# Optimization experiments

Hardware: AMD Instinct MI355X
Metric: run time of the kernel (lower is better)

The kernel has to match this reference:

```python
import jax, jax.numpy as jnp
import numpy as np

ROUTER_FEATS = 32  # per perspective

def setup_inputs() -> dict:
    key = jax.random.key(0)
    ks = jax.random.split(key, 8)
    B, L1, L2, L3, E = 16384, 3072, 15, 32, 8
    x = jax.random.normal(ks[0], (B, L1), dtype=jnp.float32)
    router_w = jax.random.normal(ks[1], (E, 2 * ROUTER_FEATS), dtype=jnp.float32) * 0.1
    router_b = jnp.zeros((E,), dtype=jnp.float32)
    l1_w = jax.random.normal(ks[2], (E, L2 + 1, L1), dtype=jnp.float32) / np.sqrt(L1)
    l1_b = jax.random.normal(ks[3], (E, L2 + 1), dtype=jnp.float32) * 0.01
    l2_w = jax.random.normal(ks[4], (E, L3, 2 * L2), dtype=jnp.float32) / np.sqrt(2 * L2)
    l2_b = jax.random.normal(ks[5], (E, L3), dtype=jnp.float32) * 0.01
    out_w = jax.random.normal(ks[6], (E, 1, L3), dtype=jnp.float32) / np.sqrt(L3)
    out_b = jnp.zeros((E, 1), dtype=jnp.float32)
    return {"x": x, "router_w": router_w, "router_b": router_b,
            "l1_w": l1_w, "l1_b": l1_b, "l2_w": l2_w, "l2_b": l2_b,
            "out_w": out_w, "out_b": out_b}

def reference(x, router_w, router_b, l1_w, l1_b, l2_w, l2_b, out_w, out_b):
    # x: [B, L1]; l1_w: [E, L2+1, L1]; l2_w: [E, L3, 2*L2]; out_w: [E, 1, L3]
    L2 = l2_w.shape[2] // 2
    half = x.shape[1] // 2
    # router: first ROUTER_FEATS features of each perspective
    router_in = jnp.concatenate([x[:, :ROUTER_FEATS], x[:, half:half + ROUTER_FEATS]], axis=1)  # [B, 64]
    gate_logits = router_in @ router_w.T + router_b  # [B, E]
    expert_indices = jnp.argmax(gate_logits, axis=-1)  # [B]
    # all-experts dense forward
    l1c = jnp.einsum('bi,eoi->beo', x, l1_w) + l1_b          # [B, E, L2+1]
    l1x, l1x_out = l1c[..., :L2], l1c[..., L2:]               # [B,E,L2], [B,E,1]
    l1x = jnp.clip(jnp.concatenate([jnp.square(l1x) * (255.0 / 256.0), l1x], axis=2), 0.0, 1.0)  # [B,E,2*L2]
    l2c = jnp.einsum('bei,eoi->beo', l1x, l2_w) + l2_b        # [B, E, L3]
    l2x = jnp.clip(l2c, 0.0, 1.0)
    l3c = jnp.einsum('bei,eoi->beo', l2x, out_w) + out_b      # [B, E, 1]
    all_outputs = l3c + l1x_out                               # [B, E, 1]
    # gather selected expert output (eval path)
    out = jnp.take_along_axis(all_outputs, expert_indices[:, None, None], axis=1)[:, 0, :]  # [B, 1]
    return out
```

## Files before the change

### kernel.cpp

```cpp
#include <hip/hip_runtime.h>
#include <cstdint>
#include <cstddef>

#define NROWS   16384
#define L1DIM   3072
#define NEXP    8
#define NO1     16
#define NFEAT   30
#define NL3     32
#define RFEAT   32

#define RPB     32
#define KC      192
#define NCHUNK  16
#define PITCH   196
#define NKS     8
#define KSL     24
#define SENT    0x7FFFFFFF
#define RBLK    256
#define MAXSLOTS (NROWS + NEXP*RPB)
#define MBLK    (MAXSLOTS/RPB)

__device__ int g_eid[NROWS];
__device__ int g_bc[RBLK*NEXP];
__device__ int g_off[NEXP+1];
__device__ int g_cur[NEXP];
__device__ int g_bucket[MAXSLOTS];

__global__ __launch_bounds__(64) void k_router(const float* __restrict__ x,
                                               const float* __restrict__ rw,
                                               const float* __restrict__ rb){
  int tid = threadIdx.x;
  int row = blockIdx.x*64 + tid;
  const float* xr = x + (size_t)row * L1DIM;
  float rin[2*RFEAT];
  #pragma unroll
  for (int i=0;i<8;i++){
    float4 v = *(const float4*)(xr + i*4);
    rin[i*4+0]=v.x; rin[i*4+1]=v.y; rin[i*4+2]=v.z; rin[i*4+3]=v.w;
  }
  #pragma unroll
  for (int i=0;i<8;i++){
    float4 v = *(const float4*)(xr + (L1DIM/2) + i*4);
    rin[32+i*4+0]=v.x; rin[32+i*4+1]=v.y; rin[32+i*4+2]=v.z; rin[32+i*4+3]=v.w;
  }
  float best = -3.0e38f; int be = 0;
  #pragma unroll
  for (int e=0;e<NEXP;e++){
    float s = rb[e];
    #pragma unroll
    for (int i=0;i<64;i++) s += rin[i]*rw[e*64+i];
    if (s > best){ best = s; be = e; }
  }
  g_eid[row] = be;
  __shared__ int cnt[NEXP];
  if (tid < NEXP) cnt[tid] = 0;
  __syncthreads();
  atomicAdd(&cnt[be], 1);
  __syncthreads();
  if (tid < NEXP) g_bc[blockIdx.x*NEXP + tid] = cnt[tid];
}

__global__ __launch_bounds__(256) void k_offsets(){
  __shared__ int part[256];
  __shared__ int scnt[NEXP];
  __shared__ int soff[NEXP+1];
  int tid = threadIdx.x;
  {
    int e = tid & 7, grp = tid >> 3;
    int s = 0;
    for (int b = grp; b < RBLK; b += 32) s += g_bc[b*NEXP + e];
    part[tid] = s;
  }
  __syncthreads();
  if (tid < NEXP){
    int t = 0;
    #pragma unroll
    for (int g=0; g<32; g++) t += part[g*NEXP + tid];
    scnt[tid] = t;
    g_cur[tid] = 0;
  }
  __syncthreads();
  if (tid == 0){
    int o = 0;
    for (int ee=0; ee<NEXP; ee++){
      soff[ee] = o;
      o += ((scnt[ee] + RPB - 1) / RPB) * RPB;
    }
    soff[NEXP] = o;
    for (int i=0;i<=NEXP;i++) g_off[i] = soff[i];
  }
  __syncthreads();
  for (int ee=0; ee<NEXP; ee++){
    int s    = soff[ee] + scnt[ee];
    int epad = soff[ee+1];
    for (int i = s + tid; i < epad; i += 256) g_bucket[i] = SENT;
  }
}

__global__ __launch_bounds__(64) void k_scatter(){
  int lane = threadIdx.x;
  int row = blockIdx.x*64 + lane;
  int e = g_eid[row];
  unsigned long long peers = 0;
  #pragma unroll
  for (int j=0;j<NEXP;j++){
    unsigned long long m = __ballot(e == j);
    if (e == j) peers = m;
  }
  int rank   = __popcll(peers & ((1ull << lane) - 1ull));
  int leader = __ffsll((unsigned long long)peers) - 1;
  int base = 0;
  if (lane == leader) base = atomicAdd(&g_cur[e], __popcll(peers));
  base = __shfl(base, leader, 64);
  g_bucket[g_off[e] + base + rank] = row;
}

__global__ __launch_bounds__(256,2) void k_main(const float* __restrict__ x,
    const float* __restrict__ l1w, const float* __restrict__ l1b,
    const float* __restrict__ l2w, const float* __restrict__ l2b,
    const float* __restrict__ ow,  const float* __restrict__ ob,
    float* __restrict__ out){
  __shared__ __align__(16) float sX[RPB][PITCH];
  __shared__ __align__(16) float sW[NO1][PITCH];
  __shared__ int sRows[RPB];
  __shared__ int sE;

  int tid = threadIdx.x;
  int slot0 = blockIdx.x * RPB;
  if (tid == 0){
    int e = -1;
    if (slot0 < g_off[NEXP]){
      #pragma unroll
      for (int j=0;j<NEXP;j++) if (slot0 >= g_off[j] && slot0 < g_off[j+1]) e = j;
    }
    sE = e;
  }
  __syncthreads();
  int e = sE;
  if (e < 0) return;
  if (tid < RPB) sRows[tid] = g_bucket[slot0 + tid];

  int ks = tid >> 5;
  int l5 = tid & 31;
  int og = l5 & 3;
  int rg = l5 >> 2;

  float acc[4][4];
  #pragma unroll
  for (int i=0;i<4;i++)
    #pragma unroll
    for (int j=0;j<4;j++) acc[i][j] = 0.f;

  const float* we = l1w + (size_t)e * (NO1 * L1DIM);

  for (int c=0;c<NCHUNK;c++){
    int kb = c * KC;
    __syncthreads();
    #pragma unroll
    for (int p=0;p<6;p++){
      int i = tid + p*256;
      int r = i / (KC/4), k4 = i % (KC/4);
      int gr = sRows[r];
      if (gr == SENT) gr = 0;
      float4 v = *(const float4*)(x + (size_t)gr * L1DIM + kb + k4*4);
      *(float4*)(&sX[r][k4*4]) = v;
    }
    #pragma unroll
    for (int p=0;p<3;p++){
      int i = tid + p*256;
      int o = i / (KC/4), k4 = i % (KC/4);
      float4 v = *(const float4*)(we + (size_t)o * L1DIM + kb + k4*4);
      *(float4*)(&sW[o][k4*4]) = v;
    }
    __syncthreads();
    int k0 = ks * KSL;
    #pragma unroll
    for (int q=0;q<KSL/4;q++){
      int k = k0 + q*4;
      float4 xv[4], wv[4];
      #pragma unroll
      for (int i=0;i<4;i++) xv[i] = *(const float4*)(&sX[rg + i*8][k]);
      #pragma unroll
      for (int j=0;j<4;j++) wv[j] = *(const float4*)(&sW[og + j*4][k]);
      #pragma unroll
      for (int ri=0;ri<4;ri++)
        #pragma unroll
        for (int oi=0;oi<4;oi++){
          acc[ri][oi] += xv[ri].x * wv[oi].x;
          acc[ri][oi] += xv[ri].y * wv[oi].y;
          acc[ri][oi] += xv[ri].z * wv[oi].z;
          acc[ri][oi] += xv[ri].w * wv[oi].w;
        }
    }
  }

  __syncthreads();
  float* red = &sX[0][0];
  #pragma unroll
  for (int ri=0;ri<4;ri++)
    #pragma unroll
    for (int oi=0;oi<4;oi++)
      red[(ks*RPB + (rg + ri*8))*17 + (og + oi*4)] = acc[ri][oi];
  __syncthreads();

  if (tid < RPB*4){
    int row = tid >> 2;
    int g   = tid & 3;
    float l1c[NO1];
    #pragma unroll
    for (int j=0;j<NO1;j++){
      float s = l1b[e*NO1 + j];
      #pragma unroll
      for (int sl=0;sl<NKS;sl++) s += red[(sl*RPB + row)*17 + j];
      l1c[j] = s;
    }
    float feat[NFEAT];
    #pragma unroll
    for (int j=0;j<15;j++){
      float v = l1c[j];
      feat[j]    = fminf(v*v*(255.0f/256.0f), 1.0f);
      feat[15+j] = fminf(fmaxf(v, 0.0f), 1.0f);
    }
    float l1xout = l1c[15];
    const float* w2 = l2w + e*NL3*NFEAT;
    const float* wo = ow  + e*NL3;
    float acc3 = 0.f;
    #pragma unroll
    for (int oo=0;oo<8;oo++){
      int o = g*8 + oo;
      float s = l2b[e*NL3 + o];
      #pragma unroll
      for (int i=0;i<NFEAT;i++) s += feat[i]*w2[o*NFEAT + i];
      s = fminf(fmaxf(s, 0.0f), 1.0f);
      acc3 += s * wo[o];
    }
    acc3 += __shfl_xor(acc3, 1);
    acc3 += __shfl_xor(acc3, 2);
    if (g == 0){
      int grow = sRows[row];
      if (grow != SENT) out[grow] = acc3 + ob[e] + l1xout;
    }
  }
}

extern "C" void kernel_launch(void* const* d_in, const int* in_sizes, int n_in,
                              void* d_out, int out_size, void* d_ws, size_t ws_size,
                              hipStream_t stream){
  (void)in_sizes; (void)n_in; (void)d_ws; (void)ws_size; (void)out_size;
  const float* x   = (const float*)d_in[0];
  const float* rw  = (const float*)d_in[1];
  const float* rb  = (const float*)d_in[2];
  const float* l1w = (const float*)d_in[3];
  const float* l1b = (const float*)d_in[4];
  const float* l2w = (const float*)d_in[5];
  const float* l2b = (const float*)d_in[6];
  const float* ow  = (const float*)d_in[7];
  const float* ob  = (const float*)d_in[8];
  float* out = (float*)d_out;

  hipLaunchKernelGGL(k_router,  dim3(RBLK), dim3(64),  0, stream, x, rw, rb);
  hipLaunchKernelGGL(k_offsets, dim3(1),    dim3(256), 0, stream);
  hipLaunchKernelGGL(k_scatter, dim3(RBLK), dim3(64),  0, stream);
  hipLaunchKernelGGL(k_main,    dim3(MBLK), dim3(256), 0, stream,
                     x, l1w, l1b, l2w, l2b, ow, ob, out);
}
```

Measured before the change: 341.2 us.

## Double-buffer main GEMM tiles via register prefetch; replace scatter atomics with prefix scan

k_main now keeps two shared-memory buffers and loads the next K-chunk of x and weights into registers while the current chunk is being multiplied. This hides global-load latency and cuts one barrier per chunk. Gather offsets are precomputed once and __launch_bounds__ loses the min-blocks hint. Separately, k_offsets computes exclusive per-block bases so k_scatter writes without global atomics. The costs are doubled LDS usage, which may lower occupancy, and extra registers for the prefetched data.

New measurement: 429.6 us. 1.26x slower.

```diff
diff --git a/kernel.cpp b/kernel.cpp
--- a/kernel.cpp
+++ b/kernel.cpp
@@ -12,6 +12,7 @@
 
 #define RPB     32
 #define KC      192
+#define KC4     48
 #define NCHUNK  16
 #define PITCH   196
 #define NKS     8
@@ -23,8 +24,8 @@
 
 __device__ int g_eid[NROWS];
 __device__ int g_bc[RBLK*NEXP];
+__device__ int g_base[RBLK*NEXP];
 __device__ int g_off[NEXP+1];
-__device__ int g_cur[NEXP];
 __device__ int g_bucket[MAXSLOTS];
 
 __global__ __launch_bounds__(64) void k_router(const float* __restrict__ x,
@@ -62,23 +63,30 @@
 }
 
 __global__ __launch_bounds__(256) void k_offsets(){
-  __shared__ int part[256];
+  __shared__ int sbc[RBLK*NEXP];
+  __shared__ int gpart[32*NEXP];
+  __shared__ int gpre[32*NEXP];
   __shared__ int scnt[NEXP];
   __shared__ int soff[NEXP+1];
   int tid = threadIdx.x;
+  #pragma unroll
+  for (int p=0;p<8;p++) sbc[tid + p*256] = g_bc[tid + p*256];
+  __syncthreads();
+  int e = tid & 7, g = tid >> 3;
   {
-    int e = tid & 7, grp = tid >> 3;
     int s = 0;
-    for (int b = grp; b < RBLK; b += 32) s += g_bc[b*NEXP + e];
-    part[tid] = s;
+    #pragma unroll
+    for (int b=0;b<8;b++) s += sbc[(g*8+b)*NEXP + e];
+    gpart[g*NEXP + e] = s;
   }
   __syncthreads();
   if (tid < NEXP){
-    int t = 0;
-    #pragma unroll
-    for (int g=0; g<32; g++) t += part[g*NEXP + tid];
-    scnt[tid] = t;
-    g_cur[tid] = 0;
+    int run = 0;
+    for (int gg=0;gg<32;gg++){
+      gpre[gg*NEXP + tid] = run;
+      run += gpart[gg*NEXP + tid];
+    }
+    scnt[tid] = run;
   }
   __syncthreads();
   if (tid == 0){
@@ -91,6 +99,14 @@
     for (int i=0;i<=NEXP;i++) g_off[i] = soff[i];
   }
   __syncthreads();
+  {
+    int run = soff[e] + gpre[g*NEXP + e];
+    #pragma unroll
+    for (int b=0;b<8;b++){
+      g_base[(g*8+b)*NEXP + e] = run;
+      run += sbc[(g*8+b)*NEXP + e];
+    }
+  }
   for (int ee=0; ee<NEXP; ee++){
     int s    = soff[ee] + scnt[ee];
     int epad = soff[ee+1];
@@ -108,21 +124,17 @@
     unsigned long long m = __ballot(e == j);
     if (e == j) peers = m;
   }
-  int rank   = __popcll(peers & ((1ull << lane) - 1ull));
-  int leader = __ffsll((unsigned long long)peers) - 1;
-  int base = 0;
-  if (lane == leader) base = atomicAdd(&g_cur[e], __popcll(peers));
-  base = __shfl(base, leader, 64);
-  g_bucket[g_off[e] + base + rank] = row;
-}
-
-__global__ __launch_bounds__(256,2) void k_main(const float* __restrict__ x,
+  int rank = __popcll(peers & ((1ull << lane) - 1ull));
+  g_bucket[g_base[blockIdx.x*NEXP + e] + rank] = row;
+}
+
+__global__ __launch_bounds__(256) void k_main(const float* __restrict__ x,
     const float* __restrict__ l1w, const float* __restrict__ l1b,
     const float* __restrict__ l2w, const float* __restrict__ l2b,
     const float* __restrict__ ow,  const float* __restrict__ ob,
     float* __restrict__ out){
-  __shared__ __align__(16) float sX[RPB][PITCH];
-  __shared__ __align__(16) float sW[NO1][PITCH];
+  __shared__ __align__(16) float sX[2][RPB][PITCH];
+  __shared__ __align__(16) float sW[2][NO1][PITCH];
   __shared__ int sRows[RPB];
   __shared__ int sE;
 
@@ -140,6 +152,25 @@
   int e = sE;
   if (e < 0) return;
   if (tid < RPB) sRows[tid] = g_bucket[slot0 + tid];
+  __syncthreads();
+
+  const char* xb = (const char*)x;
+  const char* wb = (const char*)(l1w + (size_t)e * (NO1 * L1DIM));
+
+  unsigned xgo[6], xlo[6], wgo[3], wlo[3];
+  #pragma unroll
+  for (int p=0;p<6;p++){
+    int i = tid + p*256, r = i / KC4, k4 = i % KC4;
+    int gr = sRows[r]; if (gr == SENT) gr = 0;
+    xgo[p] = (unsigned)gr * (L1DIM*4) + (unsigned)k4 * 16;
+    xlo[p] = ((unsigned)r * PITCH + (unsigned)k4 * 4) * 4;
+  }
+  #pragma unroll
+  for (int p=0;p<3;p++){
+    int i = tid + p*256, o = i / KC4, k4 = i % KC4;
+    wgo[p] = (unsigned)o * (L1DIM*4) + (unsigned)k4 * 16;
+    wlo[p] = ((unsigned)o * PITCH + (unsigned)k4 * 4) * 4;
+  }
 
   int ks = tid >> 5;
   int l5 = tid & 31;
@@ -152,37 +183,74 @@
     #pragma unroll
     for (int j=0;j<4;j++) acc[i][j] = 0.f;
 
-  const float* we = l1w + (size_t)e * (NO1 * L1DIM);
-
-  for (int c=0;c<NCHUNK;c++){
-    int kb = c * KC;
+  float4 rx[6], rw4[3];
+  char* sXb = (char*)&sX[0][0][0];
+  char* sWb = (char*)&sW[0][0][0];
+  const unsigned XBUF = RPB*PITCH*4, WBUF = NO1*PITCH*4;
+
+  #pragma unroll
+  for (int p=0;p<6;p++) rx[p]  = *(const float4*)(xb + xgo[p]);
+  #pragma unroll
+  for (int p=0;p<3;p++) rw4[p] = *(const float4*)(wb + wgo[p]);
+  #pragma unroll
+  for (int p=0;p<6;p++) *(float4*)(sXb + xlo[p]) = rx[p];
+  #pragma unroll
+  for (int p=0;p<3;p++) *(float4*)(sWb + wlo[p]) = rw4[p];
+  __syncthreads();
+
+  for (int c=0; c<NCHUNK-1; c++){
+    unsigned kb = (unsigned)(c+1) * (KC*4);
+    #pragma unroll
+    for (int p=0;p<6;p++) rx[p]  = *(const float4*)(xb + xgo[p] + kb);
+    #pragma unroll
+    for (int p=0;p<3;p++) rw4[p] = *(const float4*)(wb + wgo[p] + kb);
+    {
+      int buf = c & 1;
+      const float (*cX)[PITCH] = sX[buf];
+      const float (*cW)[PITCH] = sW[buf];
+      int k0 = ks * KSL;
+      #pragma unroll
+      for (int q=0;q<KSL/4;q++){
+        int k = k0 + q*4;
+        float4 xv[4], wv[4];
+        #pragma unroll
+        for (int i=0;i<4;i++) xv[i] = *(const float4*)(&cX[rg + i*8][k]);
+        #pragma unroll
+        for (int j=0;j<4;j++) wv[j] = *(const float4*)(&cW[og + j*4][k]);
+        #pragma unroll
+        for (int ri=0;ri<4;ri++)
+          #pragma unroll
+          for (int oi=0;oi<4;oi++){
+            acc[ri][oi] += xv[ri].x * wv[oi].x;
+            acc[ri][oi] += xv[ri].y * wv[oi].y;
+            acc[ri][oi] += xv[ri].z * wv[oi].z;
+            acc[ri][oi] += xv[ri].w * wv[oi].w;
+          }
+      }
+    }
+    {
+      unsigned bo = (unsigned)((c+1)&1);
+      char* dX = sXb + bo*XBUF;
+      char* dW = sWb + bo*WBUF;
+      #pragma unroll
+      for (int p=0;p<6;p++) *(float4*)(dX + xlo[p]) = rx[p];
+      #pragma unroll
+      for (int p=0;p<3;p++) *(float4*)(dW + wlo[p]) = rw4[p];
+    }
     __syncthreads();
-    #pragma unroll
-    for (int p=0;p<6;p++){
-      int i = tid + p*256;
-      int r = i / (KC/4), k4 = i % (KC/4);
-      int gr = sRows[r];
-      if (gr == SENT) gr = 0;
-      float4 v = *(const float4*)(x + (size_t)gr * L1DIM + kb + k4*4);
-      *(float4*)(&sX[r][k4*4]) = v;
-    }
-    #pragma unroll
-    for (int p=0;p<3;p++){
-      int i = tid + p*256;
-      int o = i / (KC/4), k4 = i % (KC/4);
-      float4 v = *(const float4*)(we + (size_t)o * L1DIM + kb + k4*4);
-      *(float4*)(&sW[o][k4*4]) = v;
-    }
-    __syncthreads();
+  }
+  {
+    const float (*cX)[PITCH] = sX[1];
+    const float (*cW)[PITCH] = sW[1];
     int k0 = ks * KSL;
     #pragma unroll
     for (int q=0;q<KSL/4;q++){
       int k = k0 + q*4;
       float4 xv[4], wv[4];
       #pragma unroll
-      for (int i=0;i<4;i++) xv[i] = *(const float4*)(&sX[rg + i*8][k]);
-      #pragma unroll
-      for (int j=0;j<4;j++) wv[j] = *(const float4*)(&sW[og + j*4][k]);
+      for (int i=0;i<4;i++) xv[i] = *(const float4*)(&cX[rg + i*8][k]);
+      #pragma unroll
+      for (int j=0;j<4;j++) wv[j] = *(const float4*)(&cW[og + j*4][k]);
       #pragma unroll
       for (int ri=0;ri<4;ri++)
         #pragma unroll
@@ -196,7 +264,7 @@
   }
 
   __syncthreads();
-  float* red = &sX[0][0];
+  float* red = &sX[0][0][0];
   #pragma unroll
   for (int ri=0;ri<4;ri++)
     #pragma unroll
```

## Restructure expert GEMM to per-wave rows with direct global x loads and shuffle reduction

Applied to the files above, without the earlier changes.

The main kernel now gives each wave 4 gathered rows and reads x straight from global memory, with no shared-memory staging. Only the expert's 16x512 weight chunk goes through LDS, and all 16 outputs are accumulated per lane. The partial sums are reduced across the wave with a 64-lane butterfly of xor shuffles, and the tail MLP is spread over 16 lanes per row. Rows per block drop from 32 to 16 and occupancy is raised to 3 blocks per CU. The scatter pass now uses per-block prefix offsets computed in k_offsets instead of global atomics. The trade-off is 64 accumulators per thread and a costly 6-step shuffle reduction over 64 values, against lower LDS traffic for x.

Result: slower. 416.3 us (+22.0%).

```diff
diff --git a/kernel.cpp b/kernel.cpp
--- a/kernel.cpp
+++ b/kernel.cpp
@@ -10,12 +10,9 @@
 #define NL3     32
 #define RFEAT   32
 
-#define RPB     32
-#define KC      192
-#define NCHUNK  16
-#define PITCH   196
-#define NKS     8
-#define KSL     24
+#define RPB     16
+#define KCH     512
+#define NCH     6
 #define SENT    0x7FFFFFFF
 #define RBLK    256
 #define MAXSLOTS (NROWS + NEXP*RPB)
@@ -23,8 +20,8 @@
 
 __device__ int g_eid[NROWS];
 __device__ int g_bc[RBLK*NEXP];
+__device__ int g_base[RBLK*NEXP];
 __device__ int g_off[NEXP+1];
-__device__ int g_cur[NEXP];
 __device__ int g_bucket[MAXSLOTS];
 
 __global__ __launch_bounds__(64) void k_router(const float* __restrict__ x,
@@ -62,23 +59,30 @@
 }
 
 __global__ __launch_bounds__(256) void k_offsets(){
-  __shared__ int part[256];
+  __shared__ int sbc[RBLK*NEXP];
+  __shared__ int gpart[32*NEXP];
+  __shared__ int gpre[32*NEXP];
   __shared__ int scnt[NEXP];
   __shared__ int soff[NEXP+1];
   int tid = threadIdx.x;
+  #pragma unroll
+  for (int p=0;p<8;p++) sbc[tid + p*256] = g_bc[tid + p*256];
+  __syncthreads();
+  int e = tid & 7, g = tid >> 3;
   {
-    int e = tid & 7, grp = tid >> 3;
     int s = 0;
-    for (int b = grp; b < RBLK; b += 32) s += g_bc[b*NEXP + e];
-    part[tid] = s;
+    #pragma unroll
+    for (int b=0;b<8;b++) s += sbc[(g*8+b)*NEXP + e];
+    gpart[g*NEXP + e] = s;
   }
   __syncthreads();
   if (tid < NEXP){
-    int t = 0;
-    #pragma unroll
-    for (int g=0; g<32; g++) t += part[g*NEXP + tid];
-    scnt[tid] = t;
-    g_cur[tid] = 0;
+    int run = 0;
+    for (int gg=0;gg<32;gg++){
+      gpre[gg*NEXP + tid] = run;
+      run += gpart[gg*NEXP + tid];
+    }
+    scnt[tid] = run;
   }
   __syncthreads();
   if (tid == 0){
@@ -91,6 +95,14 @@
     for (int i=0;i<=NEXP;i++) g_off[i] = soff[i];
   }
   __syncthreads();
+  {
+    int run = soff[e] + gpre[g*NEXP + e];
+    #pragma unroll
+    for (int b=0;b<8;b++){
+      g_base[(g*8+b)*NEXP + e] = run;
+      run += sbc[(g*8+b)*NEXP + e];
+    }
+  }
   for (int ee=0; ee<NEXP; ee++){
     int s    = soff[ee] + scnt[ee];
     int epad = soff[ee+1];
@@ -108,21 +120,16 @@
     unsigned long long m = __ballot(e == j);
     if (e == j) peers = m;
   }
-  int rank   = __popcll(peers & ((1ull << lane) - 1ull));
-  int leader = __ffsll((unsigned long long)peers) - 1;
-  int base = 0;
-  if (lane == leader) base = atomicAdd(&g_cur[e], __popcll(peers));
-  base = __shfl(base, leader, 64);
-  g_bucket[g_off[e] + base + rank] = row;
-}
-
-__global__ __launch_bounds__(256,2) void k_main(const float* __restrict__ x,
+  int rank = __popcll(peers & ((1ull << lane) - 1ull));
+  g_bucket[g_base[blockIdx.x*NEXP + e] + rank] = row;
+}
+
+__global__ __launch_bounds__(256,3) void k_main(const float* __restrict__ x,
     const float* __restrict__ l1w, const float* __restrict__ l1b,
     const float* __restrict__ l2w, const float* __restrict__ l2b,
     const float* __restrict__ ow,  const float* __restrict__ ob,
     float* __restrict__ out){
-  __shared__ __align__(16) float sX[RPB][PITCH];
-  __shared__ __align__(16) float sW[NO1][PITCH];
+  __shared__ __align__(16) float sW[NO1][KCH];
   __shared__ int sRows[RPB];
   __shared__ int sE;
 
@@ -140,107 +147,107 @@
   int e = sE;
   if (e < 0) return;
   if (tid < RPB) sRows[tid] = g_bucket[slot0 + tid];
-
-  int ks = tid >> 5;
-  int l5 = tid & 31;
-  int og = l5 & 3;
-  int rg = l5 >> 2;
-
-  float acc[4][4];
-  #pragma unroll
-  for (int i=0;i<4;i++)
-    #pragma unroll
-    for (int j=0;j<4;j++) acc[i][j] = 0.f;
-
-  const float* we = l1w + (size_t)e * (NO1 * L1DIM);
-
-  for (int c=0;c<NCHUNK;c++){
-    int kb = c * KC;
+  __syncthreads();
+
+  int lane = tid & 63;
+  int wid  = tid >> 6;
+  const char* xb = (const char*)x;
+  const char* wb = (const char*)(l1w + (size_t)e * (NO1 * L1DIM));
+  char* sWb = (char*)&sW[0][0];
+
+  unsigned xoff[4];
+  #pragma unroll
+  for (int r=0;r<4;r++){
+    int gr = sRows[wid*4 + r];
+    int use = (gr == SENT) ? 0 : gr;
+    xoff[r] = (unsigned)use * (L1DIM*4) + (unsigned)lane * 16;
+  }
+
+  float acc[4][16];
+  #pragma unroll
+  for (int r=0;r<4;r++)
+    #pragma unroll
+    for (int o=0;o<16;o++) acc[r][o] = 0.f;
+
+  for (int c=0; c<NCH; c++){
+    unsigned cb = (unsigned)c * (KCH*4);
     __syncthreads();
     #pragma unroll
-    for (int p=0;p<6;p++){
-      int i = tid + p*256;
-      int r = i / (KC/4), k4 = i % (KC/4);
-      int gr = sRows[r];
-      if (gr == SENT) gr = 0;
-      float4 v = *(const float4*)(x + (size_t)gr * L1DIM + kb + k4*4);
-      *(float4*)(&sX[r][k4*4]) = v;
-    }
-    #pragma unroll
-    for (int p=0;p<3;p++){
-      int i = tid + p*256;
-      int o = i / (KC/4), k4 = i % (KC/4);
-      float4 v = *(const float4*)(we + (size_t)o * L1DIM + kb + k4*4);
-      *(float4*)(&sW[o][k4*4]) = v;
+    for (int p=0;p<8;p++){
+      int idx = tid + p*256;
+      int o  = idx >> 7;
+      int k4 = idx & 127;
+      float4 v = *(const float4*)(wb + (unsigned)o*(L1DIM*4) + cb + (unsigned)k4*16);
+      *(float4*)(sWb + (unsigned)idx*16) = v;
     }
     __syncthreads();
-    int k0 = ks * KSL;
-    #pragma unroll
-    for (int q=0;q<KSL/4;q++){
-      int k = k0 + q*4;
-      float4 xv[4], wv[4];
-      #pragma unroll
-      for (int i=0;i<4;i++) xv[i] = *(const float4*)(&sX[rg + i*8][k]);
-      #pragma unroll
-      for (int j=0;j<4;j++) wv[j] = *(const float4*)(&sW[og + j*4][k]);
-      #pragma unroll
-      for (int ri=0;ri<4;ri++)
+    #pragma unroll
+    for (int it=0; it<2; it++){
+      float4 xv[4];
+      #pragma unroll
+      for (int r=0;r<4;r++)
+        xv[r] = *(const float4*)(xb + xoff[r] + cb + it*1024);
+      #pragma unroll
+      for (int o=0;o<16;o++){
+        float4 wv = *(const float4*)(sWb + o*(KCH*4) + it*1024 + lane*16);
         #pragma unroll
-        for (int oi=0;oi<4;oi++){
-          acc[ri][oi] += xv[ri].x * wv[oi].x;
-          acc[ri][oi] += xv[ri].y * wv[oi].y;
-          acc[ri][oi] += xv[ri].z * wv[oi].z;
-          acc[ri][oi] += xv[ri].w * wv[oi].w;
+        for (int r=0;r<4;r++){
+          acc[r][o] += xv[r].x * wv.x;
+          acc[r][o] += xv[r].y * wv.y;
+          acc[r][o] += xv[r].z * wv.z;
+          acc[r][o] += xv[r].w * wv.w;
         }
-    }
-  }
-
-  __syncthreads();
-  float* red = &sX[0][0];
-  #pragma unroll
-  for (int ri=0;ri<4;ri++)
-    #pragma unroll
-    for (int oi=0;oi<4;oi++)
-      red[(ks*RPB + (rg + ri*8))*17 + (og + oi*4)] = acc[ri][oi];
-  __syncthreads();
-
-  if (tid < RPB*4){
-    int row = tid >> 2;
-    int g   = tid & 3;
-    float l1c[NO1];
-    #pragma unroll
-    for (int j=0;j<NO1;j++){
-      float s = l1b[e*NO1 + j];
-      #pragma unroll
-      for (int sl=0;sl<NKS;sl++) s += red[(sl*RPB + row)*17 + j];
-      l1c[j] = s;
-    }
-    float feat[NFEAT];
-    #pragma unroll
-    for (int j=0;j<15;j++){
-      float v = l1c[j];
-      feat[j]    = fminf(v*v*(255.0f/256.0f), 1.0f);
-      feat[15+j] = fminf(fmaxf(v, 0.0f), 1.0f);
-    }
-    float l1xout = l1c[15];
-    const float* w2 = l2w + e*NL3*NFEAT;
-    const float* wo = ow  + e*NL3;
-    float acc3 = 0.f;
-    #pragma unroll
-    for (int oo=0;oo<8;oo++){
-      int o = g*8 + oo;
-      float s = l2b[e*NL3 + o];
-      #pragma unroll
-      for (int i=0;i<NFEAT;i++) s += feat[i]*w2[o*NFEAT + i];
-      s = fminf(fmaxf(s, 0.0f), 1.0f);
-      acc3 += s * wo[o];
-    }
-    acc3 += __shfl_xor(acc3, 1);
-    acc3 += __shfl_xor(acc3, 2);
-    if (g == 0){
-      int grow = sRows[row];
-      if (grow != SENT) out[grow] = acc3 + ob[e] + l1xout;
-    }
+      }
+    }
+  }
+
+  #pragma unroll
+  for (int m=1; m<64; m<<=1){
+    #pragma unroll
+    for (int r=0;r<4;r++)
+      #pragma unroll
+      for (int o=0;o<16;o++)
+        acc[r][o] += __shfl_xor(acc[r][o], m, 64);
+  }
+
+  int row = lane >> 4;
+  int og  = lane & 15;
+  float l1c[NO1];
+  #pragma unroll
+  for (int j=0;j<NO1;j++){
+    float v = acc[0][j];
+    if (row == 1) v = acc[1][j];
+    if (row == 2) v = acc[2][j];
+    if (row == 3) v = acc[3][j];
+    l1c[j] = v + l1b[e*NO1 + j];
+  }
+  float feat[NFEAT];
+  #pragma unroll
+  for (int j=0;j<15;j++){
+    float v = l1c[j];
+    feat[j]    = fminf(v*v*(255.0f/256.0f), 1.0f);
+    feat[15+j] = fminf(fmaxf(v, 0.0f), 1.0f);
+  }
+  float l1xout = l1c[15];
+  const float* w2 = l2w + e*NL3*NFEAT;
+  const float* wo = ow  + e*NL3;
+  float acc3 = 0.f;
+  #pragma unroll
+  for (int oo=0;oo<2;oo++){
+    int o = og*2 + oo;
+    float s = l2b[e*NL3 + o];
+    #pragma unroll
+    for (int i=0;i<NFEAT;i++) s += feat[i]*w2[o*NFEAT + i];
+    s = fminf(fmaxf(s, 0.0f), 1.0f);
+    acc3 += s * wo[o];
+  }
+  acc3 += __shfl_xor(acc3, 1);
+  acc3 += __shfl_xor(acc3, 2);
+  acc3 += __shfl_xor(acc3, 4);
+  acc3 += __shfl_xor(acc3, 8);
+  if (og == 0){
+    int gr = sRows[wid*4 + row];
+    if (gr != SENT) out[gr] = acc3 + ob[e] + l1xout;
   }
 }
 
```
